# Kernel tuning notes

Hardware: AMD Instinct MI355X
Metric: run time of the kernel (lower is better)

## Reference

```python
import jax, jax.numpy as jnp
import numpy as np

B, S, E, H = 2, 2048, 1024, 16
DH = E // H
SCALE = 1.0 / float(np.sqrt(E))  # note: original scales by 1/sqrt(hidden_dim), not head_dim


def _icl_mask(s):
    # triu(diagonal=0) is masked (-inf): only strictly-past positions visible,
    # except (0,0) which is explicitly unmasked so row 0 attends to itself.
    m = jnp.triu(jnp.ones((s, s), dtype=bool), k=0)
    return m.at[0, 0].set(False)


def setup_inputs() -> dict:
    key = jax.random.key(0)
    ks = jax.random.split(key, 7)
    mk = lambda k, shp: jax.random.normal(k, shp, dtype=jnp.float32)
    return {
        "q": mk(ks[0], (B, S, E)),
        "k": mk(ks[1], (B, S, E)),
        "v": mk(ks[2], (B, S, E)),
        "Wq": mk(ks[3], (E, E)) * 0.02,
        "Wk": mk(ks[4], (E, E)) * 0.02,
        "Wv": mk(ks[5], (E, E)) * 0.02,
        "Wo": mk(ks[6], (E, E)) * 0.02,
    }


def reference(q, k, v, Wq, Wk, Wv, Wo):
    b, s, e = q.shape
    h, dh = H, e // H
    # projections (nn.Linear: x @ W.T), split heads -> [b, h, s, dh]
    qh = (q @ Wq.T).reshape(b, s, h, dh).transpose(0, 2, 1, 3)
    kh = (k @ Wk.T).reshape(b, s, h, dh).transpose(0, 2, 1, 3)
    vh = (v @ Wv.T).reshape(b, s, h, dh).transpose(0, 2, 1, 3)
    scores = jnp.einsum("bhsd,bhtd->bhst", qh, kh) * SCALE  # [b,h,s,s]
    scores = jnp.where(_icl_mask(s), -jnp.inf, scores)
    probs = jax.nn.softmax(scores, axis=-1)
    out = jnp.einsum("bhst,bhtd->bhsd", probs, vh)
    out = out.transpose(0, 2, 1, 3).reshape(b, s, e)
    return out @ Wo.T
```

## Files before the change

### kernel.cpp

```cpp
#include <hip/hip_runtime.h>
#include <hip/hip_bf16.h>

typedef unsigned short u16;
typedef unsigned int u32;
typedef __bf16 bf16x8 __attribute__((ext_vector_type(8)));
typedef float float4_ __attribute__((ext_vector_type(4)));

#define B_ 2
#define S_ 2048
#define E_ 1024
#define H_ 16
#define DH_ 64
#define M_ (B_*S_)
#define E2_ (E_*E_)
#define SCALE_ 0.03125f
#define LOG2E_ 1.4426950408889634f

__device__ __forceinline__ u16 f2bf(float f) {
    unsigned int x = __float_as_uint(f);
    x += 0x7fffu + ((x >> 16) & 1u);
    return (u16)(x >> 16);
}

template <typename T> struct raw8;
template <> struct raw8<float> { float4_ lo, hi; };
template <> struct raw8<u16>   { bf16x8 v; };

__device__ __forceinline__ raw8<float> ldr8(const float* p) {
    raw8<float> r; const float4_* q = (const float4_*)p; r.lo = q[0]; r.hi = q[1]; return r;
}
__device__ __forceinline__ raw8<u16> ldr8(const u16* p) {
    raw8<u16> r; r.v = *(const bf16x8*)p; return r;
}
__device__ __forceinline__ bf16x8 cvt8(const raw8<u16>& r) { return r.v; }
__device__ __forceinline__ bf16x8 cvt8(const raw8<float>& r) {
    union { bf16x8 v; __hip_bfloat162 h[4]; } u;
    u.h[0] = __float22bfloat162_rn(float2{r.lo[0], r.lo[1]});
    u.h[1] = __float22bfloat162_rn(float2{r.lo[2], r.lo[3]});
    u.h[2] = __float22bfloat162_rn(float2{r.hi[0], r.hi[1]});
    u.h[3] = __float22bfloat162_rn(float2{r.hi[2], r.hi[3]});
    return u.v;
}
__device__ __forceinline__ bf16x8 ld8(const u16* p) { return *(const bf16x8*)p; }

__device__ __forceinline__ void async16(u16* lds, const u16* g) {
    __builtin_amdgcn_global_load_lds(
        (const __attribute__((address_space(1))) u32*)g,
        (__attribute__((address_space(3))) u32*)lds, 16, 0, 0);
}

__device__ __forceinline__ int swz32(int row, int col) {
    return row * 32 + ((((col >> 3) ^ (row & 3)) << 3) | (col & 7));
}

__global__ __launch_bounds__(256)
void convw_kernel(const float* __restrict__ Wq, const float* __restrict__ Wk,
                  const float* __restrict__ Wv, const float* __restrict__ Wo,
                  u16* __restrict__ Wqb, u16* __restrict__ Wkb,
                  u16* __restrict__ Wvb, u16* __restrict__ Wob) {
    const int which = blockIdx.y;
    const float* src = which == 0 ? Wq : which == 1 ? Wk : which == 2 ? Wv : Wo;
    u16* dst        = which == 0 ? Wqb : which == 1 ? Wkb : which == 2 ? Wvb : Wob;
    size_t off = ((size_t)blockIdx.x * 256 + threadIdx.x) * 8;
    *(bf16x8*)&dst[off] = cvt8(ldr8(&src[off]));
}

__global__ __launch_bounds__(256)
void convx_kernel(const float* __restrict__ q, const float* __restrict__ k,
                  const float* __restrict__ v,
                  u16* __restrict__ Xq, u16* __restrict__ Xk, u16* __restrict__ Xv) {
    const int which = blockIdx.y;
    const float* src = which == 0 ? q : which == 1 ? k : v;
    u16* dst        = which == 0 ? Xq : which == 1 ? Xk : Xv;
    size_t off = ((size_t)blockIdx.x * 256 + threadIdx.x) * 8;
    *(bf16x8*)&dst[off] = cvt8(ldr8(&src[off]));
}

__global__ __launch_bounds__(256)
void proj_kernel(const u16* __restrict__ Xq, const u16* __restrict__ Xk, const u16* __restrict__ Xv,
                 const u16* __restrict__ Wqb, const u16* __restrict__ Wkb, const u16* __restrict__ Wvb,
                 u16* __restrict__ Qh, u16* __restrict__ Kh, u16* __restrict__ Vt) {
    const int z = blockIdx.z;
    const u16* A   = (z == 0) ? Xq : (z == 1) ? Xk : Xv;
    const u16* Wb  = (z == 0) ? Wqb : (z == 1) ? Wkb : Wvb;
    u16* C         = (z == 0) ? Qh : (z == 1) ? Kh : Vt;
    const float cscale = (z == 0) ? SCALE_ : 1.0f;
    const int transV = (z == 2);
    const int bm = blockIdx.x * 128, bn = blockIdx.y * 128;

    __shared__ u16 As[2][128 * 32];
    __shared__ u16 Bs[2][128 * 32];

    const int tid  = threadIdx.x;
    const int lane = tid & 63;
    const int w    = tid >> 6;
    const int wr   = (w >> 1) * 64, wc = (w & 1) * 64;
    const int m16  = lane & 15, quad = lane >> 4, q4 = quad * 4;

    const int row0 = tid >> 2, ch = tid & 3, row1 = row0 + 64;
    const int csw  = ((ch ^ (row0 & 3)) * 8);
    const u16* ag0 = &A[(size_t)(bm + row0) * 1024 + csw];
    const u16* ag1 = &A[(size_t)(bm + row1) * 1024 + csw];
    const u16* wg0 = &Wb[(size_t)(bn + row0) * 1024 + csw];
    const u16* wg1 = &Wb[(size_t)(bn + row1) * 1024 + csw];

    float4_ acc[4][4];
#pragma unroll
    for (int i = 0; i < 4; i++)
#pragma unroll
        for (int j = 0; j < 4; j++) acc[i][j] = (float4_){0.f, 0.f, 0.f, 0.f};

    async16((u16*)((char*)As[0] + (size_t)tid * 16), ag0);
    async16((u16*)((char*)As[0] + (size_t)tid * 16 + 4096), ag1);
    async16((u16*)((char*)Bs[0] + (size_t)tid * 16), wg0);
    async16((u16*)((char*)Bs[0] + (size_t)tid * 16 + 4096), wg1);
    __syncthreads();

    auto step = [&](int t, const u16* Asc, const u16* Bsc, u16* Asn, u16* Bsn) {
        if (t < 31) {
            const size_t ko = (size_t)(t + 1) * 32;
            async16((u16*)((char*)Asn + (size_t)tid * 16), ag0 + ko);
            async16((u16*)((char*)Asn + (size_t)tid * 16 + 4096), ag1 + ko);
            async16((u16*)((char*)Bsn + (size_t)tid * 16), wg0 + ko);
            async16((u16*)((char*)Bsn + (size_t)tid * 16 + 4096), wg1 + ko);
        }
        __builtin_amdgcn_sched_barrier(0);
        bf16x8 af[4], bfr[4];
#pragma unroll
        for (int rt = 0; rt < 4; rt++)
            af[rt] = *(const bf16x8*)&Asc[swz32(wr + rt * 16 + m16, quad * 8)];
#pragma unroll
        for (int ct = 0; ct < 4; ct++)
            bfr[ct] = *(const bf16x8*)&Bsc[swz32(wc + ct * 16 + m16, quad * 8)];
#pragma unroll
        for (int rt = 0; rt < 4; rt++)
#pragma unroll
            for (int ct = 0; ct < 4; ct++)
                acc[rt][ct] = __builtin_amdgcn_mfma_f32_16x16x32_bf16(af[rt], bfr[ct], acc[rt][ct], 0, 0, 0);
        if (t < 31) __syncthreads();
    };

    for (int t = 0; t < 32; t += 2) {
        step(t,     As[0], Bs[0], As[1], Bs[1]);
        step(t + 1, As[1], Bs[1], As[0], Bs[0]);
    }

#pragma unroll
    for (int rt = 0; rt < 4; rt++)
#pragma unroll
        for (int ct = 0; ct < 4; ct++)
#pragma unroll
            for (int r = 0; r < 4; r++) {
                int row = bm + wr + rt * 16 + q4 + r;
                int col = bn + wc + ct * 16 + m16;
                u16 val = f2bf(acc[rt][ct][r] * cscale);
                if (!transV) {
                    C[(size_t)row * 1024 + col] = val;
                } else {
                    int bb = row >> 11, s = row & 2047;
                    C[((size_t)(bb * 1024 + col)) * 2048 + s] = val;
                }
            }
}

__global__ __launch_bounds__(256)
void out_kernel(const u16* __restrict__ AO, const u16* __restrict__ Wob, float* __restrict__ C) {
    const int bm = blockIdx.x * 128, bn = blockIdx.y * 64;

    __shared__ u16 As[2][128 * 32];
    __shared__ u16 Bs[2][64 * 32];

    const int tid  = threadIdx.x;
    const int lane = tid & 63;
    const int w    = tid >> 6;
    const int m16  = lane & 15, quad = lane >> 4, q4 = quad * 4;
    const int c1   = tid + 256;

    const int swc = (((tid & 3) ^ ((tid >> 2) & 3)) * 8);
    const u16* ag0 = &AO[(size_t)(bm + (tid >> 2)) * 1024 + swc];
    const u16* ag1 = &AO[(size_t)(bm + (c1 >> 2)) * 1024 + swc];
    const u16* bg  = &Wob[(size_t)(bn + (tid >> 2)) * 1024 + swc];

    float4_ acc[2][4];
#pragma unroll
    for (int i = 0; i < 2; i++)
#pragma unroll
        for (int j = 0; j < 4; j++) acc[i][j] = (float4_){0.f, 0.f, 0.f, 0.f};

    async16((u16*)((char*)As[0] + (size_t)tid * 16), ag0);
    async16((u16*)((char*)As[0] + (size_t)c1 * 16), ag1);
    async16((u16*)((char*)Bs[0] + (size_t)tid * 16), bg);
    __syncthreads();

    auto step = [&](int t, const u16* Asc, const u16* Bsc, u16* Asn, u16* Bsn) {
        if (t < 31) {
            async16((u16*)((char*)Asn + (size_t)tid * 16), ag0 + (t + 1) * 32);
            async16((u16*)((char*)Asn + (size_t)c1 * 16), ag1 + (t + 1) * 32);
            async16((u16*)((char*)Bsn + (size_t)tid * 16), bg + (t + 1) * 32);
        }
        __builtin_amdgcn_sched_barrier(0);
        bf16x8 af[2], bfr[4];
#pragma unroll
        for (int rt = 0; rt < 2; rt++)
            af[rt] = *(const bf16x8*)&Asc[swz32(w * 32 + rt * 16 + m16, quad * 8)];
#pragma unroll
        for (int ct = 0; ct < 4; ct++)
            bfr[ct] = *(const bf16x8*)&Bsc[swz32(ct * 16 + m16, quad * 8)];
#pragma unroll
        for (int rt = 0; rt < 2; rt++)
#pragma unroll
            for (int ct = 0; ct < 4; ct++)
                acc[rt][ct] = __builtin_amdgcn_mfma_f32_16x16x32_bf16(af[rt], bfr[ct], acc[rt][ct], 0, 0, 0);
        if (t < 31) __syncthreads();
    };

    for (int t = 0; t < 32; t += 2) {
        step(t,     As[0], Bs[0], As[1], Bs[1]);
        step(t + 1, As[1], Bs[1], As[0], Bs[0]);
    }

#pragma unroll
    for (int rt = 0; rt < 2; rt++)
#pragma unroll
        for (int ct = 0; ct < 4; ct++)
#pragma unroll
            for (int r = 0; r < 4; r++) {
                int row = bm + w * 32 + rt * 16 + q4 + r;
                int col = bn + ct * 16 + m16;
                C[(size_t)row * 1024 + col] = acc[rt][ct][r];
            }
}

__device__ __forceinline__ int sw64(int row, int col) {
    return row * 64 + ((((col >> 3) ^ (row & 7)) << 3) | (col & 7));
}

__global__ __launch_bounds__(512)
void attn_kernel(const u16* __restrict__ Qh, const u16* __restrict__ Kh,
                 const u16* __restrict__ Vt, u16* __restrict__ O) {
    const int h    = blockIdx.x;
    const int pair = blockIdx.y;
    const int b    = blockIdx.z;
    const int tqA  = pair;
    const int tqB  = 31 - pair;
    const int tid  = threadIdx.x;
    const int lane = tid & 63;
    const int w    = tid >> 6;
    const int half = w >> 2;
    const int w4   = w & 3;
    const int myTq = half ? tqB : tqA;
    const int m16  = lane & 15;
    const int quad = lane >> 4;
    const int q4   = quad * 4;

    __shared__ u16 Ks[2][64 * 64];
    __shared__ u16 Vs[2][64 * 64];
    __shared__ u16 Ps[2][64 * 64];

    const int srow = tid >> 3;
    const int skc  = (tid & 7) * 8;
    const int sblk = ((skc >> 3) ^ (srow & 7)) << 3;

    const size_t kbase = ((size_t)(b * S_)) * E_ + h * DH_;
    const size_t vbase = ((size_t)(b * 1024 + h * DH_)) * 2048;

    bf16x8 qf[2];
    {
        const u16* qa = Qh + ((size_t)(b * S_ + myTq * 64 + w4 * 16 + m16)) * E_ + h * DH_;
        qf[0] = ld8(qa + quad * 8);
        qf[1] = ld8(qa + 32 + quad * 8);
    }

    float l_part[4] = {0.f, 0.f, 0.f, 0.f};
    float4_ o_acc[4];
#pragma unroll
    for (int dt = 0; dt < 4; dt++) o_acc[dt] = (float4_){0.f, 0.f, 0.f, 0.f};

    *(bf16x8*)&Ks[0][srow * 64 + sblk] = ld8(&Kh[kbase + (size_t)srow * E_ + skc]);
    *(bf16x8*)&Vs[0][srow * 64 + sblk] = ld8(&Vt[vbase + (size_t)srow * 2048 + skc]);
    __syncthreads();

    for (int t = 0; t <= tqB; t++) {
        const int cur = t & 1;

        bf16x8 kr, vr;
        const bool havepf = (t < tqB);
        if (havepf) {
            kr = ld8(&Kh[kbase + (size_t)((t + 1) * 64 + srow) * E_ + skc]);
            vr = ld8(&Vt[vbase + (size_t)srow * 2048 + (t + 1) * 64 + skc]);
        }

        if (t <= myTq) {
            const u16* Kc = &Ks[cur][0];
            const u16* Vc = &Vs[cur][0];
            u16* Pm = &Ps[half][0];

            float4_ sc[4];
#pragma unroll
            for (int ct = 0; ct < 4; ct++) sc[ct] = (float4_){0.f, 0.f, 0.f, 0.f};
#pragma unroll
            for (int ks = 0; ks < 2; ks++)
#pragma unroll
                for (int ct = 0; ct < 4; ct++) {
                    bf16x8 kf = *(const bf16x8*)&Kc[sw64(ct * 16 + m16, ks * 32 + quad * 8)];
                    sc[ct] = __builtin_amdgcn_mfma_f32_16x16x32_bf16(qf[ks], kf, sc[ct], 0, 0, 0);
                }

            float p[4][4];
            if (t != myTq) {
#pragma unroll
                for (int ct = 0; ct < 4; ct++)
#pragma unroll
                    for (int r = 0; r < 4; r++) {
                        float pp = exp2f(sc[ct][r] * LOG2E_);
                        p[ct][r] = pp;
                        l_part[r] += pp;
                    }
            } else {
#pragma unroll
                for (int ct = 0; ct < 4; ct++)
#pragma unroll
                    for (int r = 0; r < 4; r++) {
                        int i_loc = w4 * 16 + q4 + r;
                        int j_loc = ct * 16 + m16;
                        bool allow = (j_loc < i_loc) || (myTq == 0 && i_loc == 0 && j_loc == 0);
                        float pp = allow ? exp2f(sc[ct][r] * LOG2E_) : 0.f;
                        p[ct][r] = pp;
                        l_part[r] += pp;
                    }
            }

#pragma unroll
            for (int ct = 0; ct < 4; ct++)
#pragma unroll
                for (int r = 0; r < 4; r++)
                    Pm[sw64(w4 * 16 + q4 + r, ct * 16 + m16)] = f2bf(p[ct][r]);

#pragma unroll
            for (int ks = 0; ks < 2; ks++) {
                bf16x8 pf = *(const bf16x8*)&Pm[sw64(w4 * 16 + m16, ks * 32 + quad * 8)];
#pragma unroll
                for (int dt = 0; dt < 4; dt++) {
                    bf16x8 vf = *(const bf16x8*)&Vc[sw64(dt * 16 + m16, ks * 32 + quad * 8)];
                    o_acc[dt] = __builtin_amdgcn_mfma_f32_16x16x32_bf16(pf, vf, o_acc[dt], 0, 0, 0);
                }
            }
        }

        if (havepf) {
            const int nxt = cur ^ 1;
            *(bf16x8*)&Ks[nxt][srow * 64 + sblk] = kr;
            *(bf16x8*)&Vs[nxt][srow * 64 + sblk] = vr;
        }
        __syncthreads();
    }

    const size_t obase = ((size_t)(b * S_ + myTq * 64)) * E_ + h * DH_;
#pragma unroll
    for (int r = 0; r < 4; r++) {
        float l = l_part[r];
#pragma unroll
        for (int msk = 1; msk <= 8; msk <<= 1) l += __shfl_xor(l, msk);
        float inv_l = 1.0f / l;
        int row = w4 * 16 + q4 + r;
#pragma unroll
        for (int dt = 0; dt < 4; dt++) {
            int col = dt * 16 + m16;
            O[obase + (size_t)row * E_ + col] = f2bf(o_acc[dt][r] * inv_l);
        }
    }
}

extern "C" void kernel_launch(void* const* d_in, const int* in_sizes, int n_in,
                              void* d_out, int out_size, void* d_ws, size_t ws_size,
                              hipStream_t stream) {
    const float* q  = (const float*)d_in[0];
    const float* k  = (const float*)d_in[1];
    const float* v  = (const float*)d_in[2];
    const float* Wq = (const float*)d_in[3];
    const float* Wk = (const float*)d_in[4];
    const float* Wv = (const float*)d_in[5];
    const float* Wo = (const float*)d_in[6];

    const size_t ME = (size_t)M_ * E_;
    u16* ws  = (u16*)d_ws;
    u16* Qh  = ws;
    u16* Kh  = ws + ME;
    u16* Vt  = ws + 2 * ME;
    u16* AO  = ws + 3 * ME;
    u16* Wqb = AO;
    u16* Wkb = AO + E2_;
    u16* Wvb = AO + 2 * (size_t)E2_;
    u16* Wob = ws + 4 * ME;
    u16* Xv  = ws + 4 * ME + E2_;
    u16* Xq  = (u16*)d_out;
    u16* Xk  = Xq + ME;

    dim3 blk(256);
    convw_kernel<<<dim3(512, 4), blk, 0, stream>>>(Wq, Wk, Wv, Wo, Wqb, Wkb, Wvb, Wob);
    convx_kernel<<<dim3(2048, 3), blk, 0, stream>>>(q, k, v, Xq, Xk, Xv);
    proj_kernel<<<dim3(32, 8, 3), blk, 0, stream>>>(Xq, Xk, Xv, Wqb, Wkb, Wvb, Qh, Kh, Vt);
    attn_kernel<<<dim3(16, 16, 2), dim3(512), 0, stream>>>(Qh, Kh, Vt, AO);
    out_kernel<<<dim3(32, 16), blk, 0, stream>>>(AO, Wob, (float*)d_out);
}
```

Baseline: 216.2 us.

## Split attention KV tiles across wave groups instead of query tiles, then reduce

Each block previously gave one 64-row query tile to each group of four waves, so the group owning the short tile sat idle while the other finished the long KV loop. Now both groups hold both query tiles and take alternating KV tiles, two per iteration. Their partial outputs and row sums are combined through shared memory at the end, which balances the load between groups. It adds double Q and accumulator registers, an extra barrier per step, a final cross-group reduction, and a launch-bounds occupancy hint that may push the compiler to spill.

```diff
diff --git a/kernel.cpp b/kernel.cpp
--- a/kernel.cpp
+++ b/kernel.cpp
@@ -235,7 +235,7 @@
     return row * 64 + ((((col >> 3) ^ (row & 7)) << 3) | (col & 7));
 }
 
-__global__ __launch_bounds__(512)
+__global__ __launch_bounds__(512, 4)
 void attn_kernel(const u16* __restrict__ Qh, const u16* __restrict__ Kh,
                  const u16* __restrict__ Vt, u16* __restrict__ O) {
     const int h    = blockIdx.x;
@@ -246,9 +246,8 @@
     const int tid  = threadIdx.x;
     const int lane = tid & 63;
     const int w    = tid >> 6;
-    const int half = w >> 2;
+    const int grp  = w >> 2;
     const int w4   = w & 3;
-    const int myTq = half ? tqB : tqA;
     const int m16  = lane & 15;
     const int quad = lane >> 4;
     const int q4   = quad * 4;
@@ -260,113 +259,168 @@
     const int srow = tid >> 3;
     const int skc  = (tid & 7) * 8;
     const int sblk = ((skc >> 3) ^ (srow & 7)) << 3;
+    const int sdst = srow * 64 + sblk;
 
     const size_t kbase = ((size_t)(b * S_)) * E_ + h * DH_;
     const size_t vbase = ((size_t)(b * 1024 + h * DH_)) * 2048;
 
-    bf16x8 qf[2];
+    bf16x8 qfA[2], qfB[2];
     {
-        const u16* qa = Qh + ((size_t)(b * S_ + myTq * 64 + w4 * 16 + m16)) * E_ + h * DH_;
-        qf[0] = ld8(qa + quad * 8);
-        qf[1] = ld8(qa + 32 + quad * 8);
-    }
-
-    float l_part[4] = {0.f, 0.f, 0.f, 0.f};
-    float4_ o_acc[4];
-#pragma unroll
-    for (int dt = 0; dt < 4; dt++) o_acc[dt] = (float4_){0.f, 0.f, 0.f, 0.f};
-
-    *(bf16x8*)&Ks[0][srow * 64 + sblk] = ld8(&Kh[kbase + (size_t)srow * E_ + skc]);
-    *(bf16x8*)&Vs[0][srow * 64 + sblk] = ld8(&Vt[vbase + (size_t)srow * 2048 + skc]);
-    __syncthreads();
-
-    for (int t = 0; t <= tqB; t++) {
-        const int cur = t & 1;
-
-        bf16x8 kr, vr;
-        const bool havepf = (t < tqB);
-        if (havepf) {
-            kr = ld8(&Kh[kbase + (size_t)((t + 1) * 64 + srow) * E_ + skc]);
-            vr = ld8(&Vt[vbase + (size_t)srow * 2048 + (t + 1) * 64 + skc]);
-        }
-
-        if (t <= myTq) {
-            const u16* Kc = &Ks[cur][0];
-            const u16* Vc = &Vs[cur][0];
-            u16* Pm = &Ps[half][0];
-
-            float4_ sc[4];
-#pragma unroll
-            for (int ct = 0; ct < 4; ct++) sc[ct] = (float4_){0.f, 0.f, 0.f, 0.f};
-#pragma unroll
-            for (int ks = 0; ks < 2; ks++)
-#pragma unroll
-                for (int ct = 0; ct < 4; ct++) {
-                    bf16x8 kf = *(const bf16x8*)&Kc[sw64(ct * 16 + m16, ks * 32 + quad * 8)];
-                    sc[ct] = __builtin_amdgcn_mfma_f32_16x16x32_bf16(qf[ks], kf, sc[ct], 0, 0, 0);
+        const u16* qa = Qh + ((size_t)(b * S_ + tqA * 64 + w4 * 16 + m16)) * E_ + h * DH_;
+        const u16* qb = Qh + ((size_t)(b * S_ + tqB * 64 + w4 * 16 + m16)) * E_ + h * DH_;
+        qfA[0] = ld8(qa + quad * 8);  qfA[1] = ld8(qa + 32 + quad * 8);
+        qfB[0] = ld8(qb + quad * 8);  qfB[1] = ld8(qb + 32 + quad * 8);
+    }
+
+    float lA[4] = {0.f, 0.f, 0.f, 0.f}, lB[4] = {0.f, 0.f, 0.f, 0.f};
+    float4_ oA[4], oB[4];
+#pragma unroll
+    for (int dt = 0; dt < 4; dt++) { oA[dt] = (float4_){0.f,0.f,0.f,0.f}; oB[dt] = (float4_){0.f,0.f,0.f,0.f}; }
+
+    *(bf16x8*)&Ks[0][sdst] = ld8(&Kh[kbase + (size_t)srow * E_ + skc]);
+    *(bf16x8*)&Vs[0][sdst] = ld8(&Vt[vbase + (size_t)srow * 2048 + skc]);
+    *(bf16x8*)&Ks[1][sdst] = ld8(&Kh[kbase + (size_t)(64 + srow) * E_ + skc]);
+    *(bf16x8*)&Vs[1][sdst] = ld8(&Vt[vbase + (size_t)srow * 2048 + 64 + skc]);
+    __syncthreads();
+
+    auto process = [&](const bf16x8* qf, float* l_part, float4_* o_acc, int tqX, int kt) {
+        const u16* Kc = &Ks[grp][0];
+        const u16* Vc = &Vs[grp][0];
+        u16* Pm = &Ps[grp][0];
+        float4_ sc[4];
+#pragma unroll
+        for (int ct = 0; ct < 4; ct++) sc[ct] = (float4_){0.f, 0.f, 0.f, 0.f};
+#pragma unroll
+        for (int ks = 0; ks < 2; ks++)
+#pragma unroll
+            for (int ct = 0; ct < 4; ct++) {
+                bf16x8 kf = *(const bf16x8*)&Kc[sw64(ct * 16 + m16, ks * 32 + quad * 8)];
+                sc[ct] = __builtin_amdgcn_mfma_f32_16x16x32_bf16(qf[ks], kf, sc[ct], 0, 0, 0);
+            }
+
+        if (kt != tqX) {
+#pragma unroll
+            for (int ct = 0; ct < 4; ct++)
+#pragma unroll
+                for (int r = 0; r < 4; r++) {
+                    float pp = exp2f(sc[ct][r] * LOG2E_);
+                    l_part[r] += pp;
+                    Pm[sw64(w4 * 16 + q4 + r, ct * 16 + m16)] = f2bf(pp);
                 }
-
-            float p[4][4];
-            if (t != myTq) {
-#pragma unroll
-                for (int ct = 0; ct < 4; ct++)
-#pragma unroll
-                    for (int r = 0; r < 4; r++) {
-                        float pp = exp2f(sc[ct][r] * LOG2E_);
-                        p[ct][r] = pp;
-                        l_part[r] += pp;
-                    }
-            } else {
-#pragma unroll
-                for (int ct = 0; ct < 4; ct++)
-#pragma unroll
-                    for (int r = 0; r < 4; r++) {
-                        int i_loc = w4 * 16 + q4 + r;
-                        int j_loc = ct * 16 + m16;
-                        bool allow = (j_loc < i_loc) || (myTq == 0 && i_loc == 0 && j_loc == 0);
-                        float pp = allow ? exp2f(sc[ct][r] * LOG2E_) : 0.f;
-                        p[ct][r] = pp;
-                        l_part[r] += pp;
-                    }
+        } else {
+#pragma unroll
+            for (int ct = 0; ct < 4; ct++)
+#pragma unroll
+                for (int r = 0; r < 4; r++) {
+                    int i_loc = w4 * 16 + q4 + r;
+                    int j_loc = ct * 16 + m16;
+                    bool allow = (j_loc < i_loc) || (tqX == 0 && i_loc == 0 && j_loc == 0);
+                    float pp = allow ? exp2f(sc[ct][r] * LOG2E_) : 0.f;
+                    l_part[r] += pp;
+                    Pm[sw64(w4 * 16 + q4 + r, ct * 16 + m16)] = f2bf(pp);
+                }
+        }
+
+#pragma unroll
+        for (int ks = 0; ks < 2; ks++) {
+            bf16x8 pf = *(const bf16x8*)&Pm[sw64(w4 * 16 + m16, ks * 32 + quad * 8)];
+#pragma unroll
+            for (int dt = 0; dt < 4; dt++) {
+                bf16x8 vf = *(const bf16x8*)&Vc[sw64(dt * 16 + m16, ks * 32 + quad * 8)];
+                o_acc[dt] = __builtin_amdgcn_mfma_f32_16x16x32_bf16(pf, vf, o_acc[dt], 0, 0, 0);
             }
-
-#pragma unroll
-            for (int ct = 0; ct < 4; ct++)
-#pragma unroll
-                for (int r = 0; r < 4; r++)
-                    Pm[sw64(w4 * 16 + q4 + r, ct * 16 + m16)] = f2bf(p[ct][r]);
-
-#pragma unroll
-            for (int ks = 0; ks < 2; ks++) {
-                bf16x8 pf = *(const bf16x8*)&Pm[sw64(w4 * 16 + m16, ks * 32 + quad * 8)];
-#pragma unroll
-                for (int dt = 0; dt < 4; dt++) {
-                    bf16x8 vf = *(const bf16x8*)&Vc[sw64(dt * 16 + m16, ks * 32 + quad * 8)];
-                    o_acc[dt] = __builtin_amdgcn_mfma_f32_16x16x32_bf16(pf, vf, o_acc[dt], 0, 0, 0);
-                }
+        }
+    };
+
+    for (int kt2 = 0; kt2 <= tqB; kt2 += 2) {
+        bf16x8 kr0, kr1, vr0, vr1;
+        const bool pf0 = (kt2 + 2 <= tqB);
+        const bool pf1 = (kt2 + 3 <= tqB);
+        if (pf0) {
+            kr0 = ld8(&Kh[kbase + (size_t)((kt2 + 2) * 64 + srow) * E_ + skc]);
+            vr0 = ld8(&Vt[vbase + (size_t)srow * 2048 + (kt2 + 2) * 64 + skc]);
+        }
+        if (pf1) {
+            kr1 = ld8(&Kh[kbase + (size_t)((kt2 + 3) * 64 + srow) * E_ + skc]);
+            vr1 = ld8(&Vt[vbase + (size_t)srow * 2048 + (kt2 + 3) * 64 + skc]);
+        }
+
+        const int kt = kt2 + grp;
+        if (kt <= tqB) {
+            process(qfB, lB, oB, tqB, kt);
+            if (kt <= tqA) process(qfA, lA, oA, tqA, kt);
+        }
+
+        __syncthreads();
+        if (pf0) { *(bf16x8*)&Ks[0][sdst] = kr0; *(bf16x8*)&Vs[0][sdst] = vr0; }
+        if (pf1) { *(bf16x8*)&Ks[1][sdst] = kr1; *(bf16x8*)&Vs[1][sdst] = vr1; }
+        __syncthreads();
+    }
+
+    float* ox = reinterpret_cast<float*>(&Ks[0][0]);
+    float* lx = reinterpret_cast<float*>(&Vs[0][0]);
+
+    if (grp == 1) {
+#pragma unroll
+        for (int dt = 0; dt < 4; dt++)
+#pragma unroll
+            for (int r = 0; r < 4; r++)
+                ox[(w4 * 16 + q4 + r) * 64 + dt * 16 + m16] = oA[dt][r];
+#pragma unroll
+        for (int r = 0; r < 4; r++)
+            lx[(w4 * 16 + q4 + r) * 16 + m16] = lA[r];
+    }
+    __syncthreads();
+    if (grp == 0) {
+#pragma unroll
+        for (int dt = 0; dt < 4; dt++)
+#pragma unroll
+            for (int r = 0; r < 4; r++)
+                oA[dt][r] += ox[(w4 * 16 + q4 + r) * 64 + dt * 16 + m16];
+#pragma unroll
+        for (int r = 0; r < 4; r++)
+            lA[r] += lx[(w4 * 16 + q4 + r) * 16 + m16];
+    }
+    __syncthreads();
+    if (grp == 0) {
+#pragma unroll
+        for (int dt = 0; dt < 4; dt++)
+#pragma unroll
+            for (int r = 0; r < 4; r++)
+                ox[(w4 * 16 + q4 + r) * 64 + dt * 16 + m16] = oB[dt][r];
+#pragma unroll
+        for (int r = 0; r < 4; r++)
+            lx[(w4 * 16 + q4 + r) * 16 + m16] = lB[r];
+    }
+    __syncthreads();
+    if (grp == 1) {
+#pragma unroll
+        for (int dt = 0; dt < 4; dt++)
+#pragma unroll
+            for (int r = 0; r < 4; r++)
+                oB[dt][r] += ox[(w4 * 16 + q4 + r) * 64 + dt * 16 + m16];
+#pragma unroll
+        for (int r = 0; r < 4; r++)
+            lB[r] += lx[(w4 * 16 + q4 + r) * 16 + m16];
+    }
+
+    {
+        const float4_* o_acc = (grp == 0) ? oA : oB;
+        const float*   l_par = (grp == 0) ? lA : lB;
+        const int      tqX   = (grp == 0) ? tqA : tqB;
+        const size_t obase = ((size_t)(b * S_ + tqX * 64)) * E_ + h * DH_;
+#pragma unroll
+        for (int r = 0; r < 4; r++) {
+            float l = l_par[r];
+#pragma unroll
+            for (int msk = 1; msk <= 8; msk <<= 1) l += __shfl_xor(l, msk);
+            float inv_l = 1.0f / l;
+            int row = w4 * 16 + q4 + r;
+#pragma unroll
+            for (int dt = 0; dt < 4; dt++) {
+                int col = dt * 16 + m16;
+                O[obase + (size_t)row * E_ + col] = f2bf(o_acc[dt][r] * inv_l);
             }
-        }
-
-        if (havepf) {
-            const int nxt = cur ^ 1;
-            *(bf16x8*)&Ks[nxt][srow * 64 + sblk] = kr;
-            *(bf16x8*)&Vs[nxt][srow * 64 + sblk] = vr;
-        }
-        __syncthreads();
-    }
-
-    const size_t obase = ((size_t)(b * S_ + myTq * 64)) * E_ + h * DH_;
-#pragma unroll
-    for (int r = 0; r < 4; r++) {
-        float l = l_part[r];
-#pragma unroll
-        for (int msk = 1; msk <= 8; msk <<= 1) l += __shfl_xor(l, msk);
-        float inv_l = 1.0f / l;
-        int row = w4 * 16 + q4 + r;
-#pragma unroll
-        for (int dt = 0; dt < 4; dt++) {
-            int col = dt * 16 + m16;
-            O[obase + (size_t)row * E_ + col] = f2bf(o_acc[dt][r] * inv_l);
         }
     }
 }
```

Result: slower. 320.9 us (+48.4%).

## Split attention into one-tile blocks with async LDS copies, heaviest tiles first

Applied to the files above, without the earlier changes.

Replaces the paired-tile 512-thread attention block with 256-thread blocks that each handle one 64-row query tile, launched heaviest-first (tq = 31 - blockIdx.y). K/V tiles are now moved global-to-LDS with async16 copies, double-buffered, in place of register-staged prefetch. Blocks are smaller and occupancy hints are set to 4, so idle half-blocks disappear and scheduling balances better across CUs. The async copies drop the swizzle on the store side and swizzle the global source address instead, which depends on async16 semantics defined elsewhere in the file.

```diff
diff --git a/kernel.cpp b/kernel.cpp
--- a/kernel.cpp
+++ b/kernel.cpp
@@ -235,38 +235,37 @@
     return row * 64 + ((((col >> 3) ^ (row & 7)) << 3) | (col & 7));
 }
 
-__global__ __launch_bounds__(512)
+__global__ __launch_bounds__(256, 4)
 void attn_kernel(const u16* __restrict__ Qh, const u16* __restrict__ Kh,
                  const u16* __restrict__ Vt, u16* __restrict__ O) {
     const int h    = blockIdx.x;
-    const int pair = blockIdx.y;
+    const int tq   = 31 - blockIdx.y;
     const int b    = blockIdx.z;
-    const int tqA  = pair;
-    const int tqB  = 31 - pair;
     const int tid  = threadIdx.x;
     const int lane = tid & 63;
     const int w    = tid >> 6;
-    const int half = w >> 2;
-    const int w4   = w & 3;
-    const int myTq = half ? tqB : tqA;
     const int m16  = lane & 15;
     const int quad = lane >> 4;
     const int q4   = quad * 4;
 
     __shared__ u16 Ks[2][64 * 64];
     __shared__ u16 Vs[2][64 * 64];
-    __shared__ u16 Ps[2][64 * 64];
-
-    const int srow = tid >> 3;
-    const int skc  = (tid & 7) * 8;
-    const int sblk = ((skc >> 3) ^ (srow & 7)) << 3;
+    __shared__ u16 Ps[64 * 64];
+
+    const int srow0 = tid >> 3;
+    const int srow1 = srow0 + 32;
+    const int ssw   = (((tid & 7) ^ (srow0 & 7)) * 8);
 
     const size_t kbase = ((size_t)(b * S_)) * E_ + h * DH_;
     const size_t vbase = ((size_t)(b * 1024 + h * DH_)) * 2048;
+    const u16* kg0 = &Kh[kbase + (size_t)srow0 * E_ + ssw];
+    const u16* kg1 = kg0 + (size_t)32 * E_;
+    const u16* vg0 = &Vt[vbase + (size_t)srow0 * 2048 + ssw];
+    const u16* vg1 = vg0 + (size_t)32 * 2048;
 
     bf16x8 qf[2];
     {
-        const u16* qa = Qh + ((size_t)(b * S_ + myTq * 64 + w4 * 16 + m16)) * E_ + h * DH_;
+        const u16* qa = Qh + ((size_t)(b * S_ + tq * 64 + w * 16 + m16)) * E_ + h * DH_;
         qf[0] = ld8(qa + quad * 8);
         qf[1] = ld8(qa + 32 + quad * 8);
     }
@@ -276,93 +275,81 @@
 #pragma unroll
     for (int dt = 0; dt < 4; dt++) o_acc[dt] = (float4_){0.f, 0.f, 0.f, 0.f};
 
-    *(bf16x8*)&Ks[0][srow * 64 + sblk] = ld8(&Kh[kbase + (size_t)srow * E_ + skc]);
-    *(bf16x8*)&Vs[0][srow * 64 + sblk] = ld8(&Vt[vbase + (size_t)srow * 2048 + skc]);
+    async16((u16*)((char*)Ks[0] + (size_t)tid * 16), kg0);
+    async16((u16*)((char*)Ks[0] + (size_t)(tid + 256) * 16), kg1);
+    async16((u16*)((char*)Vs[0] + (size_t)tid * 16), vg0);
+    async16((u16*)((char*)Vs[0] + (size_t)(tid + 256) * 16), vg1);
     __syncthreads();
 
-    for (int t = 0; t <= tqB; t++) {
-        const int cur = t & 1;
-
-        bf16x8 kr, vr;
-        const bool havepf = (t < tqB);
-        if (havepf) {
-            kr = ld8(&Kh[kbase + (size_t)((t + 1) * 64 + srow) * E_ + skc]);
-            vr = ld8(&Vt[vbase + (size_t)srow * 2048 + (t + 1) * 64 + skc]);
-        }
-
-        if (t <= myTq) {
-            const u16* Kc = &Ks[cur][0];
-            const u16* Vc = &Vs[cur][0];
-            u16* Pm = &Ps[half][0];
-
-            float4_ sc[4];
-#pragma unroll
-            for (int ct = 0; ct < 4; ct++) sc[ct] = (float4_){0.f, 0.f, 0.f, 0.f};
-#pragma unroll
-            for (int ks = 0; ks < 2; ks++)
-#pragma unroll
-                for (int ct = 0; ct < 4; ct++) {
-                    bf16x8 kf = *(const bf16x8*)&Kc[sw64(ct * 16 + m16, ks * 32 + quad * 8)];
-                    sc[ct] = __builtin_amdgcn_mfma_f32_16x16x32_bf16(qf[ks], kf, sc[ct], 0, 0, 0);
+    for (int t = 0; t <= tq; t++) {
+        const int buf = t & 1;
+        if (t < tq) {
+            const size_t ko = (size_t)(t + 1) * 64 * E_;
+            const int    vo = (t + 1) * 64;
+            async16((u16*)((char*)Ks[buf ^ 1] + (size_t)tid * 16), kg0 + ko);
+            async16((u16*)((char*)Ks[buf ^ 1] + (size_t)(tid + 256) * 16), kg1 + ko);
+            async16((u16*)((char*)Vs[buf ^ 1] + (size_t)tid * 16), vg0 + vo);
+            async16((u16*)((char*)Vs[buf ^ 1] + (size_t)(tid + 256) * 16), vg1 + vo);
+        }
+        __builtin_amdgcn_sched_barrier(0);
+
+        const u16* Kc = &Ks[buf][0];
+        const u16* Vc = &Vs[buf][0];
+
+        float4_ sc[4];
+#pragma unroll
+        for (int ct = 0; ct < 4; ct++) sc[ct] = (float4_){0.f, 0.f, 0.f, 0.f};
+#pragma unroll
+        for (int ks = 0; ks < 2; ks++)
+#pragma unroll
+            for (int ct = 0; ct < 4; ct++) {
+                bf16x8 kf = *(const bf16x8*)&Kc[sw64(ct * 16 + m16, ks * 32 + quad * 8)];
+                sc[ct] = __builtin_amdgcn_mfma_f32_16x16x32_bf16(qf[ks], kf, sc[ct], 0, 0, 0);
+            }
+
+        if (t != tq) {
+#pragma unroll
+            for (int ct = 0; ct < 4; ct++)
+#pragma unroll
+                for (int r = 0; r < 4; r++) {
+                    float pp = exp2f(sc[ct][r] * LOG2E_);
+                    l_part[r] += pp;
+                    Ps[sw64(w * 16 + q4 + r, ct * 16 + m16)] = f2bf(pp);
                 }
-
-            float p[4][4];
-            if (t != myTq) {
-#pragma unroll
-                for (int ct = 0; ct < 4; ct++)
-#pragma unroll
-                    for (int r = 0; r < 4; r++) {
-                        float pp = exp2f(sc[ct][r] * LOG2E_);
-                        p[ct][r] = pp;
-                        l_part[r] += pp;
-                    }
-            } else {
-#pragma unroll
-                for (int ct = 0; ct < 4; ct++)
-#pragma unroll
-                    for (int r = 0; r < 4; r++) {
-                        int i_loc = w4 * 16 + q4 + r;
-                        int j_loc = ct * 16 + m16;
-                        bool allow = (j_loc < i_loc) || (myTq == 0 && i_loc == 0 && j_loc == 0);
-                        float pp = allow ? exp2f(sc[ct][r] * LOG2E_) : 0.f;
-                        p[ct][r] = pp;
-                        l_part[r] += pp;
-                    }
+        } else {
+#pragma unroll
+            for (int ct = 0; ct < 4; ct++)
+#pragma unroll
+                for (int r = 0; r < 4; r++) {
+                    int i_loc = w * 16 + q4 + r;
+                    int j_loc = ct * 16 + m16;
+                    bool allow = (j_loc < i_loc) || (tq == 0 && i_loc == 0 && j_loc == 0);
+                    float pp = allow ? exp2f(sc[ct][r] * LOG2E_) : 0.f;
+                    l_part[r] += pp;
+                    Ps[sw64(w * 16 + q4 + r, ct * 16 + m16)] = f2bf(pp);
+                }
+        }
+
+#pragma unroll
+        for (int ks = 0; ks < 2; ks++) {
+            bf16x8 pf = *(const bf16x8*)&Ps[sw64(w * 16 + m16, ks * 32 + quad * 8)];
+#pragma unroll
+            for (int dt = 0; dt < 4; dt++) {
+                bf16x8 vf = *(const bf16x8*)&Vc[sw64(dt * 16 + m16, ks * 32 + quad * 8)];
+                o_acc[dt] = __builtin_amdgcn_mfma_f32_16x16x32_bf16(pf, vf, o_acc[dt], 0, 0, 0);
             }
-
-#pragma unroll
-            for (int ct = 0; ct < 4; ct++)
-#pragma unroll
-                for (int r = 0; r < 4; r++)
-                    Pm[sw64(w4 * 16 + q4 + r, ct * 16 + m16)] = f2bf(p[ct][r]);
-
-#pragma unroll
-            for (int ks = 0; ks < 2; ks++) {
-                bf16x8 pf = *(const bf16x8*)&Pm[sw64(w4 * 16 + m16, ks * 32 + quad * 8)];
-#pragma unroll
-                for (int dt = 0; dt < 4; dt++) {
-                    bf16x8 vf = *(const bf16x8*)&Vc[sw64(dt * 16 + m16, ks * 32 + quad * 8)];
-                    o_acc[dt] = __builtin_amdgcn_mfma_f32_16x16x32_bf16(pf, vf, o_acc[dt], 0, 0, 0);
-                }
-            }
-        }
-
-        if (havepf) {
-            const int nxt = cur ^ 1;
-            *(bf16x8*)&Ks[nxt][srow * 64 + sblk] = kr;
-            *(bf16x8*)&Vs[nxt][srow * 64 + sblk] = vr;
         }
         __syncthreads();
     }
 
-    const size_t obase = ((size_t)(b * S_ + myTq * 64)) * E_ + h * DH_;
+    const size_t obase = ((size_t)(b * S_ + tq * 64)) * E_ + h * DH_;
 #pragma unroll
     for (int r = 0; r < 4; r++) {
         float l = l_part[r];
 #pragma unroll
         for (int msk = 1; msk <= 8; msk <<= 1) l += __shfl_xor(l, msk);
         float inv_l = 1.0f / l;
-        int row = w4 * 16 + q4 + r;
+        int row = w * 16 + q4 + r;
 #pragma unroll
         for (int dt = 0; dt < 4; dt++) {
             int col = dt * 16 + m16;
@@ -400,6 +387,6 @@
     convw_kernel<<<dim3(512, 4), blk, 0, stream>>>(Wq, Wk, Wv, Wo, Wqb, Wkb, Wvb, Wob);
     convx_kernel<<<dim3(2048, 3), blk, 0, stream>>>(q, k, v, Xq, Xk, Xv);
     proj_kernel<<<dim3(32, 8, 3), blk, 0, stream>>>(Xq, Xk, Xv, Wqb, Wkb, Wvb, Qh, Kh, Vt);
-    attn_kernel<<<dim3(16, 16, 2), dim3(512), 0, stream>>>(Qh, Kh, Vt, AO);
+    attn_kernel<<<dim3(16, 32, 2), blk, 0, stream>>>(Qh, Kh, Vt, AO);
     out_kernel<<<dim3(32, 16), blk, 0, stream>>>(AO, Wob, (float*)d_out);
 }
```

New measurement: 218.4 us. No clear change (+1.0%).
